# Performance work log

Hardware: AMD Instinct MI355X
Metric: run time of the kernel (lower is better)

## Reference

```python
import jax, jax.numpy as jnp
import numpy as np


def setup_inputs() -> dict:
    key = jax.random.key(0)
    ks = jax.random.split(key, 8)
    B, L, I, H, O = 512, 512, 256, 1024, 1
    def glorot(k, shape, fan_sum):
        return jax.random.uniform(k, shape, jnp.float32, -1.0, 1.0) * (6.0 / fan_sum) ** 0.5
    return {
        "X": jax.random.normal(ks[0], (B, L, I), jnp.float32),
        "W_in1": glorot(ks[1], (H, I), H + I),
        "b_in1": jnp.zeros((H, 1), jnp.float32),
        "W_rec1": glorot(ks[2], (H, H), H + H),
        "W_in2": glorot(ks[3], (H, I), H + I),
        "b_in2": jnp.zeros((H, 1), jnp.float32),
        "W_rec2": glorot(ks[4], (H, H), H + H),
        "W_out": glorot(ks[5], (O, H), O + H),
        "b_out": jnp.zeros((O, 1), jnp.float32),
    }


def reference(X, W_in1, b_in1, W_rec1, W_in2, b_in2, W_rec2, W_out, b_out):
    B, L, I = X.shape
    H = W_in1.shape[0]
    Xs = jnp.swapaxes(X, 0, 1)  # (L, B, I)
    # Precompute the input-to-hidden projections for all timesteps (parallel GEMMs).
    in1 = jnp.einsum("hi,lbi->lbh", W_in1, Xs) + b_in1[:, 0]  # (L, B, H)
    in2 = jnp.einsum("hi,lbi->lbh", W_in2, Xs) + b_in2[:, 0]  # (L, B, H)
    even = (jnp.arange(L) % 2 == 0)[:, None, None]  # (L, 1, 1) broadcast mask

    def step(carry, xs):
        z12, z1, z2 = carry  # each (B, H)
        a1, a2, ev = xs
        z1n = jnp.tanh(a1 + z12 @ W_rec1.T)
        z2n = jnp.where(ev, jnp.tanh(a2 + z2 @ W_rec2.T), z2)  # branch updates only on even l
        return (z1n + z2n, z1n, z2n), None

    z0 = jnp.zeros((B, H), X.dtype)
    (z12, z1, z2), _ = jax.lax.scan(step, (z0, z0, z0), (in1, in2, even))
    z_out = jnp.tanh(z1 @ W_out.T + b_out[:, 0])  # (B, num_outputs)
    return z_out.reshape(B, 1)
```

## Files before the change

### kernel.cpp

```cpp
#include <hip/hip_runtime.h>
#include <hip/hip_bf16.h>

typedef __attribute__((ext_vector_type(8))) short bhalf8;
typedef __attribute__((ext_vector_type(4))) float fvec4;
typedef __attribute__((ext_vector_type(4))) unsigned u32x4;

static __device__ __forceinline__ unsigned short f2bf(float f) {
  unsigned u = __builtin_bit_cast(unsigned, f);
  u = (u + 0x7fffu + ((u >> 16) & 1u)) >> 16;
  return (unsigned short)u;
}
static __device__ __forceinline__ float tanh_fast(float x) {
  x = fminf(12.f, fmaxf(-12.f, x));
  float e = __expf(2.f * x);
  return (e - 1.f) / (e + 1.f);
}
static __device__ __forceinline__ fvec4 tanh4(fvec4 v) {
  fvec4 r;
  r[0] = tanh_fast(v[0]); r[1] = tanh_fast(v[1]);
  r[2] = tanh_fast(v[2]); r[3] = tanh_fast(v[3]);
  return r;
}
static __device__ __forceinline__ bhalf8 load_w8(const float* p) {
  fvec4 a = *(const fvec4*)p;
  fvec4 b = *(const fvec4*)(p + 4);
  bhalf8 r;
  r[0] = (short)f2bf(a[0]); r[1] = (short)f2bf(a[1]);
  r[2] = (short)f2bf(a[2]); r[3] = (short)f2bf(a[3]);
  r[4] = (short)f2bf(b[0]); r[5] = (short)f2bf(b[1]);
  r[6] = (short)f2bf(b[2]); r[7] = (short)f2bf(b[3]);
  return r;
}

static __device__ __forceinline__ void st_short_coh(unsigned short* p, unsigned v) {
  asm volatile("global_store_short %0, %1, off sc0 sc1" :: "v"(p), "v"(v) : "memory");
}
static __device__ __forceinline__ void st_f32_coh(float* p, float v) {
  asm volatile("global_store_dword %0, %1, off sc0 sc1" :: "v"(p), "v"(v) : "memory");
}
static __device__ __forceinline__ void st_u32_coh(unsigned* p, unsigned v) {
  asm volatile("global_store_dword %0, %1, off sc0 sc1" :: "v"(p), "v"(v) : "memory");
}
static __device__ __forceinline__ u32x4 ld16_coh(const void* p) {
  u32x4 v;
  asm volatile("global_load_dwordx4 %0, %1, off sc0 sc1" : "=v"(v) : "v"(p) : "memory");
  return v;
}
static __device__ __forceinline__ unsigned ld_u32_coh(const unsigned* p) {
  unsigned v;
  asm volatile("global_load_dword %0, %1, off sc0 sc1\n\ts_waitcnt vmcnt(0)"
               : "=v"(v) : "v"(p) : "memory");
  return v;
}
static __device__ __forceinline__ float ld_f32_coh(const float* p) {
  float v;
  asm volatile("global_load_dword %0, %1, off sc0 sc1\n\ts_waitcnt vmcnt(0)"
               : "=v"(v) : "v"(p) : "memory");
  return v;
}

#define MFMA16(a, b, c) __builtin_amdgcn_mfma_f32_16x16x32_bf16((a), (b), (c), 0, 0, 0)

extern "C" __global__ void __launch_bounds__(256, 1)
alarm_rnn_persist(const float* __restrict__ X, const float* __restrict__ Win1,
                  const float* __restrict__ bin1, const float* __restrict__ Wrec1,
                  const float* __restrict__ Win2, const float* __restrict__ bin2,
                  const float* __restrict__ Wrec2, const float* __restrict__ Wout,
                  const float* __restrict__ bout, float* __restrict__ out,
                  unsigned* flags, unsigned short* gbuf0, unsigned short* gbuf1,
                  unsigned short* z2b0, unsigned short* z2b1, float* z1buf)
{
  constexpr int kL = 512, kI = 256, kH = 1024;
  extern __shared__ char smem[];

  const int tid = threadIdx.x, bid = blockIdx.x;
  const int grp = bid >> 4, memb = bid & 15;
  const int lane = tid & 63;
  const int row16 = lane & 15, kq = lane >> 4;
  const int hcol = memb * 64 + (tid >> 6) * 16 + row16;
  const int brow0 = grp * 32;

  bhalf8 w1[32], w2[32], wi1[8], wi2[8];
  {
    const float* p1 = Wrec1 + (size_t)hcol * kH + kq * 8;
    const float* p2 = Wrec2 + (size_t)hcol * kH + kq * 8;
#pragma unroll
    for (int kk = 0; kk < 32; ++kk) {
      w1[kk] = load_w8(p1 + kk * 32);
      w2[kk] = load_w8(p2 + kk * 32);
    }
    const float* q1 = Win1 + (size_t)hcol * kI + kq * 8;
    const float* q2 = Win2 + (size_t)hcol * kI + kq * 8;
#pragma unroll
    for (int kk = 0; kk < 8; ++kk) {
      wi1[kk] = load_w8(q1 + kk * 32);
      wi2[kk] = load_w8(q2 + kk * 32);
    }
  }
  const float bv1 = bin1[hcol];
  const float bv2 = bin2[hcol];
  fvec4 z2r0 = {0.f, 0.f, 0.f, 0.f}, z2r1 = {0.f, 0.f, 0.f, 0.f};

  {
    int r = tid >> 3, q = tid & 7;
    const float* xp = X + (size_t)(brow0 + r) * (kL * kI);
    fvec4 xv[8];
#pragma unroll
    for (int j = 0; j < 8; ++j) xv[j] = *(const fvec4*)(xp + q * 4 + j * 32);
#pragma unroll
    for (int j = 0; j < 8; ++j) {
      int i0 = q * 4 + j * 32;
      ushort4 pk;
      pk.x = f2bf(xv[j][0]); pk.y = f2bf(xv[j][1]);
      pk.z = f2bf(xv[j][2]); pk.w = f2bf(xv[j][3]);
      *(ushort4*)(smem + 65536 + (r << 9) + ((i0 * 2) ^ ((r & 7) << 4))) = pk;
    }
  }

  for (int l = 0; l < kL; ++l) {
    const bool even = ((l & 1) == 0);
    const int e = l >> 1;

    {
      const unsigned short* zsrc = (l & 1) ? gbuf1 : gbuf0;
      u32x4 tmp[16];
#pragma unroll
      for (int it = 0; it < 16; ++it) {
        int c = it * 256 + tid;
        int r = c >> 7, cb = (c & 127) * 16;
        tmp[it] = ld16_coh((const char*)zsrc + (((size_t)(brow0 + r)) << 11) + cb);
      }
      asm volatile("s_waitcnt vmcnt(0)" ::: "memory");
      __builtin_amdgcn_sched_barrier(0);
#pragma unroll
      for (int it = 0; it < 16; ++it) {
        int c = it * 256 + tid;
        int r = c >> 7, cb = (c & 127) * 16;
        *(u32x4*)(smem + (r << 11) + (cb ^ ((r & 7) << 4))) = tmp[it];
      }
    }
    if (even) {
      const unsigned short* z2src = (e & 1) ? z2b1 : z2b0;
      u32x4 tmp[16];
#pragma unroll
      for (int it = 0; it < 16; ++it) {
        int c = it * 256 + tid;
        int r = c >> 7, cb = (c & 127) * 16;
        tmp[it] = ld16_coh((const char*)z2src + (((size_t)(brow0 + r)) << 11) + cb);
      }
      asm volatile("s_waitcnt vmcnt(0)" ::: "memory");
      __builtin_amdgcn_sched_barrier(0);
#pragma unroll
      for (int it = 0; it < 16; ++it) {
        int c = it * 256 + tid;
        int r = c >> 7, cb = (c & 127) * 16;
        *(u32x4*)(smem + 81920 + (r << 11) + (cb ^ ((r & 7) << 4))) = tmp[it];
      }
    }
    __syncthreads();

    const int sw = (row16 & 7) << 4;

    fvec4 acc0 = {bv1, bv1, bv1, bv1}, acc1 = acc0;
#pragma unroll
    for (int kk = 0; kk < 8; ++kk) {
      int cb = kk * 64 + kq * 16;
      bhalf8 a0 = *(const bhalf8*)(smem + 65536 + (row16 << 9) + (cb ^ sw));
      bhalf8 a1 = *(const bhalf8*)(smem + 65536 + ((16 + row16) << 9) + (cb ^ sw));
      acc0 = MFMA16(a0, wi1[kk], acc0);
      acc1 = MFMA16(a1, wi1[kk], acc1);
    }
#pragma unroll
    for (int kk = 0; kk < 32; ++kk) {
      int cb = kk * 64 + kq * 16;
      bhalf8 a0 = *(const bhalf8*)(smem + (row16 << 11) + (cb ^ sw));
      bhalf8 a1 = *(const bhalf8*)(smem + ((16 + row16) << 11) + (cb ^ sw));
      acc0 = MFMA16(a0, w1[kk], acc0);
      acc1 = MFMA16(a1, w1[kk], acc1);
    }
    fvec4 z1n0 = tanh4(acc0), z1n1 = tanh4(acc1);

    if (even) {
      fvec4 bacc0 = {bv2, bv2, bv2, bv2}, bacc1 = bacc0;
#pragma unroll
      for (int kk = 0; kk < 8; ++kk) {
        int cb = kk * 64 + kq * 16;
        bhalf8 a0 = *(const bhalf8*)(smem + 65536 + (row16 << 9) + (cb ^ sw));
        bhalf8 a1 = *(const bhalf8*)(smem + 65536 + ((16 + row16) << 9) + (cb ^ sw));
        bacc0 = MFMA16(a0, wi2[kk], bacc0);
        bacc1 = MFMA16(a1, wi2[kk], bacc1);
      }
#pragma unroll
      for (int kk = 0; kk < 32; ++kk) {
        int cb = kk * 64 + kq * 16;
        bhalf8 a0 = *(const bhalf8*)(smem + 81920 + (row16 << 11) + (cb ^ sw));
        bhalf8 a1 = *(const bhalf8*)(smem + 81920 + ((16 + row16) << 11) + (cb ^ sw));
        bacc0 = MFMA16(a0, w2[kk], bacc0);
        bacc1 = MFMA16(a1, w2[kk], bacc1);
      }
      z2r0 = tanh4(bacc0);
      z2r1 = tanh4(bacc1);
      unsigned short* z2dst = (e & 1) ? z2b0 : z2b1;
#pragma unroll
      for (int i = 0; i < 4; ++i) {
        st_short_coh(z2dst + (size_t)(brow0 + kq * 4 + i) * kH + hcol, f2bf(z2r0[i]));
        st_short_coh(z2dst + (size_t)(brow0 + 16 + kq * 4 + i) * kH + hcol, f2bf(z2r1[i]));
      }
    }

    if (l < kL - 1) {
      unsigned short* dst = (l & 1) ? gbuf0 : gbuf1;
#pragma unroll
      for (int i = 0; i < 4; ++i) {
        st_short_coh(dst + (size_t)(brow0 + kq * 4 + i) * kH + hcol, f2bf(z1n0[i] + z2r0[i]));
        st_short_coh(dst + (size_t)(brow0 + 16 + kq * 4 + i) * kH + hcol, f2bf(z1n1[i] + z2r1[i]));
      }
    } else {
#pragma unroll
      for (int i = 0; i < 4; ++i) {
        st_f32_coh(z1buf + (size_t)(brow0 + kq * 4 + i) * kH + hcol, z1n0[i]);
        st_f32_coh(z1buf + (size_t)(brow0 + 16 + kq * 4 + i) * kH + hcol, z1n1[i]);
      }
    }

    asm volatile("s_waitcnt vmcnt(0)" ::: "memory");
    __syncthreads();
    if (tid == 0) st_u32_coh(flags + grp * 16 + memb, (unsigned)(l + 1));

    fvec4 xv[8];
    const int xr = tid >> 3, xq = tid & 7;
    if (l + 1 < kL) {
      const float* xp = X + (size_t)(brow0 + xr) * (kL * kI) + (size_t)(l + 1) * kI;
#pragma unroll
      for (int j = 0; j < 8; ++j) xv[j] = *(const fvec4*)(xp + xq * 4 + j * 32);
    }

    {
      const unsigned tgt = (unsigned)(l + 1);
      const unsigned* fp = flags + grp * 16 + (lane & 15);
      for (;;) {
        unsigned v = (lane < 16) ? ld_u32_coh(fp) : tgt;
        bool ok = (lane >= 16) || ((lane & 15) == memb) || (v >= tgt);
        if (__all(ok)) break;
        __builtin_amdgcn_s_sleep(1);
      }
      __builtin_amdgcn_sched_barrier(0);
    }

    if (l + 1 < kL) {
#pragma unroll
      for (int j = 0; j < 8; ++j) {
        int i0 = xq * 4 + j * 32;
        ushort4 pk;
        pk.x = f2bf(xv[j][0]); pk.y = f2bf(xv[j][1]);
        pk.z = f2bf(xv[j][2]); pk.w = f2bf(xv[j][3]);
        *(ushort4*)(smem + 65536 + (xr << 9) + ((i0 * 2) ^ ((xr & 7) << 4))) = pk;
      }
    }
  }

  if (memb == 0) {
    int r = tid >> 3, q = tid & 7;
    const float* zr = z1buf + (size_t)(brow0 + r) * kH;
    float s = 0.f;
    for (int h = q * 128; h < q * 128 + 128; ++h) s += ld_f32_coh(zr + h) * Wout[h];
    s += __shfl_xor(s, 1);
    s += __shfl_xor(s, 2);
    s += __shfl_xor(s, 4);
    if (q == 0) out[brow0 + r] = tanh_fast(s + bout[0]);
  }
}

extern "C" void kernel_launch(void* const* d_in, const int* in_sizes, int n_in,
                              void* d_out, int out_size, void* d_ws, size_t ws_size,
                              hipStream_t stream) {
  const float* X = (const float*)d_in[0];
  const float* Win1 = (const float*)d_in[1];
  const float* bin1 = (const float*)d_in[2];
  const float* Wrec1 = (const float*)d_in[3];
  const float* Win2 = (const float*)d_in[4];
  const float* bin2 = (const float*)d_in[5];
  const float* Wrec2 = (const float*)d_in[6];
  const float* Wout = (const float*)d_in[7];
  const float* bout = (const float*)d_in[8];
  float* out = (float*)d_out;

  char* ws = (char*)d_ws;
  unsigned* flags = (unsigned*)ws;
  unsigned short* gbuf0 = (unsigned short*)(ws + 4096);
  unsigned short* gbuf1 = (unsigned short*)(ws + 4096 + (1 << 20));
  unsigned short* z2b0 = (unsigned short*)(ws + 4096 + (2 << 20));
  unsigned short* z2b1 = (unsigned short*)(ws + 4096 + (3 << 20));
  float* z1buf = (float*)(ws + 4096 + (4 << 20));

  (void)hipMemsetAsync(flags, 0, 4096, stream);
  (void)hipMemsetAsync(gbuf0, 0, (size_t)512 * 1024 * 2, stream);
  (void)hipMemsetAsync(z2b0, 0, (size_t)512 * 1024 * 2, stream);

  (void)hipFuncSetAttribute((const void*)alarm_rnn_persist,
                            hipFuncAttributeMaxDynamicSharedMemorySize, 147456);

  alarm_rnn_persist<<<dim3(256), dim3(256), 147456, stream>>>(
      X, Win1, bin1, Wrec1, Win2, bin2, Wrec2, Wout, bout, out,
      flags, gbuf0, gbuf1, z2b0, z2b1, z1buf);
}
```

Before: 6.243 ms.

## Move branch-2 recurrence off critical path into post-flag slack of odd steps

The z2 branch update for the next even step is now computed during odd steps, after the step's flag is published and before the spin-wait. This hides branch-2 work behind the cross-block barrier latency. The first z2 is computed before the loop from the input projection alone, since z2 starts at zero. X slices are double-buffered two steps ahead, and the z1 input-projection MFMAs overlap the global load of the recurrent state. Shared memory grows to 160 KB and the z2 memset is removed.

```diff
diff --git a/kernel.cpp b/kernel.cpp
--- a/kernel.cpp
+++ b/kernel.cpp
@@ -77,6 +77,7 @@
   const int grp = bid >> 4, memb = bid & 15;
   const int lane = tid & 63;
   const int row16 = lane & 15, kq = lane >> 4;
+  const int sw = (row16 & 7) << 4;
   const int hcol = memb * 64 + (tid >> 6) * 16 + row16;
   const int brow0 = grp * 32;
 
@@ -99,77 +100,78 @@
   }
   const float bv1 = bin1[hcol];
   const float bv2 = bin2[hcol];
-  fvec4 z2r0 = {0.f, 0.f, 0.f, 0.f}, z2r1 = {0.f, 0.f, 0.f, 0.f};
 
   {
     int r = tid >> 3, q = tid & 7;
-    const float* xp = X + (size_t)(brow0 + r) * (kL * kI);
-    fvec4 xv[8];
-#pragma unroll
-    for (int j = 0; j < 8; ++j) xv[j] = *(const fvec4*)(xp + q * 4 + j * 32);
-#pragma unroll
-    for (int j = 0; j < 8; ++j) {
-      int i0 = q * 4 + j * 32;
-      ushort4 pk;
-      pk.x = f2bf(xv[j][0]); pk.y = f2bf(xv[j][1]);
-      pk.z = f2bf(xv[j][2]); pk.w = f2bf(xv[j][3]);
-      *(ushort4*)(smem + 65536 + (r << 9) + ((i0 * 2) ^ ((r & 7) << 4))) = pk;
-    }
-  }
-
-  for (int l = 0; l < kL; ++l) {
-    const bool even = ((l & 1) == 0);
-    const int e = l >> 1;
-
-    {
-      const unsigned short* zsrc = (l & 1) ? gbuf1 : gbuf0;
-      u32x4 tmp[16];
-#pragma unroll
-      for (int it = 0; it < 16; ++it) {
-        int c = it * 256 + tid;
-        int r = c >> 7, cb = (c & 127) * 16;
-        tmp[it] = ld16_coh((const char*)zsrc + (((size_t)(brow0 + r)) << 11) + cb);
-      }
-      asm volatile("s_waitcnt vmcnt(0)" ::: "memory");
-      __builtin_amdgcn_sched_barrier(0);
-#pragma unroll
-      for (int it = 0; it < 16; ++it) {
-        int c = it * 256 + tid;
-        int r = c >> 7, cb = (c & 127) * 16;
-        *(u32x4*)(smem + (r << 11) + (cb ^ ((r & 7) << 4))) = tmp[it];
-      }
-    }
-    if (even) {
-      const unsigned short* z2src = (e & 1) ? z2b1 : z2b0;
-      u32x4 tmp[16];
-#pragma unroll
-      for (int it = 0; it < 16; ++it) {
-        int c = it * 256 + tid;
-        int r = c >> 7, cb = (c & 127) * 16;
-        tmp[it] = ld16_coh((const char*)z2src + (((size_t)(brow0 + r)) << 11) + cb);
-      }
-      asm volatile("s_waitcnt vmcnt(0)" ::: "memory");
-      __builtin_amdgcn_sched_barrier(0);
-#pragma unroll
-      for (int it = 0; it < 16; ++it) {
-        int c = it * 256 + tid;
-        int r = c >> 7, cb = (c & 127) * 16;
-        *(u32x4*)(smem + 81920 + (r << 11) + (cb ^ ((r & 7) << 4))) = tmp[it];
-      }
-    }
-    __syncthreads();
-
-    const int sw = (row16 & 7) << 4;
-
-    fvec4 acc0 = {bv1, bv1, bv1, bv1}, acc1 = acc0;
+#pragma unroll
+    for (int p = 0; p < 2; ++p) {
+      const float* xp = X + (size_t)(brow0 + r) * (kL * kI) + (size_t)p * kI;
+      fvec4 xv[8];
+#pragma unroll
+      for (int j = 0; j < 8; ++j) xv[j] = *(const fvec4*)(xp + q * 4 + j * 32);
+#pragma unroll
+      for (int j = 0; j < 8; ++j) {
+        int i0 = q * 4 + j * 32;
+        ushort4 pk;
+        pk.x = f2bf(xv[j][0]); pk.y = f2bf(xv[j][1]);
+        pk.z = f2bf(xv[j][2]); pk.w = f2bf(xv[j][3]);
+        *(ushort4*)(smem + 65536 + p * 16384 + (r << 9) + ((i0 * 2) ^ ((r & 7) << 4))) = pk;
+      }
+    }
+  }
+  __syncthreads();
+  fvec4 z2c0, z2c1;
+  {
+    fvec4 b0 = {bv2, bv2, bv2, bv2}, b1 = b0;
 #pragma unroll
     for (int kk = 0; kk < 8; ++kk) {
       int cb = kk * 64 + kq * 16;
       bhalf8 a0 = *(const bhalf8*)(smem + 65536 + (row16 << 9) + (cb ^ sw));
       bhalf8 a1 = *(const bhalf8*)(smem + 65536 + ((16 + row16) << 9) + (cb ^ sw));
+      b0 = MFMA16(a0, wi2[kk], b0);
+      b1 = MFMA16(a1, wi2[kk], b1);
+    }
+    z2c0 = tanh4(b0);
+    z2c1 = tanh4(b1);
+#pragma unroll
+    for (int i = 0; i < 4; ++i) {
+      st_short_coh(z2b0 + (size_t)(brow0 + kq * 4 + i) * kH + hcol, f2bf(z2c0[i]));
+      st_short_coh(z2b0 + (size_t)(brow0 + 16 + kq * 4 + i) * kH + hcol, f2bf(z2c1[i]));
+    }
+  }
+
+  for (int l = 0; l < kL; ++l) {
+    u32x4 ztmp[16];
+    {
+      const unsigned short* zsrc = (l & 1) ? gbuf1 : gbuf0;
+#pragma unroll
+      for (int it = 0; it < 16; ++it) {
+        int c = it * 256 + tid;
+        int r = c >> 7, cb = (c & 127) * 16;
+        ztmp[it] = ld16_coh((const char*)zsrc + (((size_t)(brow0 + r)) << 11) + cb);
+      }
+    }
+    const char* xb = smem + 65536 + ((l & 1) << 14);
+    fvec4 acc0 = {bv1, bv1, bv1, bv1}, acc1 = acc0;
+#pragma unroll
+    for (int kk = 0; kk < 8; ++kk) {
+      int cb = kk * 64 + kq * 16;
+      bhalf8 a0 = *(const bhalf8*)(xb + (row16 << 9) + (cb ^ sw));
+      bhalf8 a1 = *(const bhalf8*)(xb + ((16 + row16) << 9) + (cb ^ sw));
       acc0 = MFMA16(a0, wi1[kk], acc0);
       acc1 = MFMA16(a1, wi1[kk], acc1);
     }
+    __builtin_amdgcn_sched_barrier(0);
+    asm volatile("s_waitcnt vmcnt(0)" ::: "memory");
+    __builtin_amdgcn_sched_barrier(0);
+#pragma unroll
+    for (int it = 0; it < 16; ++it) {
+      int c = it * 256 + tid;
+      int r = c >> 7, cb = (c & 127) * 16;
+      *(u32x4*)(smem + (r << 11) + (cb ^ ((r & 7) << 4))) = ztmp[it];
+    }
+    __syncthreads();
+
 #pragma unroll
     for (int kk = 0; kk < 32; ++kk) {
       int cb = kk * 64 + kq * 16;
@@ -180,40 +182,12 @@
     }
     fvec4 z1n0 = tanh4(acc0), z1n1 = tanh4(acc1);
 
-    if (even) {
-      fvec4 bacc0 = {bv2, bv2, bv2, bv2}, bacc1 = bacc0;
-#pragma unroll
-      for (int kk = 0; kk < 8; ++kk) {
-        int cb = kk * 64 + kq * 16;
-        bhalf8 a0 = *(const bhalf8*)(smem + 65536 + (row16 << 9) + (cb ^ sw));
-        bhalf8 a1 = *(const bhalf8*)(smem + 65536 + ((16 + row16) << 9) + (cb ^ sw));
-        bacc0 = MFMA16(a0, wi2[kk], bacc0);
-        bacc1 = MFMA16(a1, wi2[kk], bacc1);
-      }
-#pragma unroll
-      for (int kk = 0; kk < 32; ++kk) {
-        int cb = kk * 64 + kq * 16;
-        bhalf8 a0 = *(const bhalf8*)(smem + 81920 + (row16 << 11) + (cb ^ sw));
-        bhalf8 a1 = *(const bhalf8*)(smem + 81920 + ((16 + row16) << 11) + (cb ^ sw));
-        bacc0 = MFMA16(a0, w2[kk], bacc0);
-        bacc1 = MFMA16(a1, w2[kk], bacc1);
-      }
-      z2r0 = tanh4(bacc0);
-      z2r1 = tanh4(bacc1);
-      unsigned short* z2dst = (e & 1) ? z2b0 : z2b1;
-#pragma unroll
-      for (int i = 0; i < 4; ++i) {
-        st_short_coh(z2dst + (size_t)(brow0 + kq * 4 + i) * kH + hcol, f2bf(z2r0[i]));
-        st_short_coh(z2dst + (size_t)(brow0 + 16 + kq * 4 + i) * kH + hcol, f2bf(z2r1[i]));
-      }
-    }
-
     if (l < kL - 1) {
       unsigned short* dst = (l & 1) ? gbuf0 : gbuf1;
 #pragma unroll
       for (int i = 0; i < 4; ++i) {
-        st_short_coh(dst + (size_t)(brow0 + kq * 4 + i) * kH + hcol, f2bf(z1n0[i] + z2r0[i]));
-        st_short_coh(dst + (size_t)(brow0 + 16 + kq * 4 + i) * kH + hcol, f2bf(z1n1[i] + z2r1[i]));
+        st_short_coh(dst + (size_t)(brow0 + kq * 4 + i) * kH + hcol, f2bf(z1n0[i] + z2c0[i]));
+        st_short_coh(dst + (size_t)(brow0 + 16 + kq * 4 + i) * kH + hcol, f2bf(z1n1[i] + z2c1[i]));
       }
     } else {
 #pragma unroll
@@ -222,17 +196,83 @@
         st_f32_coh(z1buf + (size_t)(brow0 + 16 + kq * 4 + i) * kH + hcol, z1n1[i]);
       }
     }
-
     asm volatile("s_waitcnt vmcnt(0)" ::: "memory");
     __syncthreads();
     if (tid == 0) st_u32_coh(flags + grp * 16 + memb, (unsigned)(l + 1));
 
     fvec4 xv[8];
     const int xr = tid >> 3, xq = tid & 7;
-    if (l + 1 < kL) {
-      const float* xp = X + (size_t)(brow0 + xr) * (kL * kI) + (size_t)(l + 1) * kI;
+    if (l + 2 < kL) {
+      const float* xp = X + (size_t)(brow0 + xr) * (kL * kI) + (size_t)(l + 2) * kI;
 #pragma unroll
       for (int j = 0; j < 8; ++j) xv[j] = *(const fvec4*)(xp + xq * 4 + j * 32);
+    }
+
+    if ((l & 1) && l < kL - 1) {
+      const int e = (l - 1) >> 1;
+      const unsigned short* z2src = (e & 1) ? z2b1 : z2b0;
+      u32x4 zt[16];
+#pragma unroll
+      for (int it = 0; it < 16; ++it) {
+        int c = it * 256 + tid;
+        int r = c >> 7, cb = (c & 127) * 16;
+        zt[it] = ld16_coh((const char*)z2src + (((size_t)(brow0 + r)) << 11) + cb);
+      }
+      const char* xb1 = smem + 65536 + (((l + 1) & 1) << 14);
+      fvec4 b0 = {bv2, bv2, bv2, bv2}, b1 = b0;
+#pragma unroll
+      for (int kk = 0; kk < 8; ++kk) {
+        int cb = kk * 64 + kq * 16;
+        bhalf8 a0 = *(const bhalf8*)(xb1 + (row16 << 9) + (cb ^ sw));
+        bhalf8 a1 = *(const bhalf8*)(xb1 + ((16 + row16) << 9) + (cb ^ sw));
+        b0 = MFMA16(a0, wi2[kk], b0);
+        b1 = MFMA16(a1, wi2[kk], b1);
+      }
+      __builtin_amdgcn_sched_barrier(0);
+      asm volatile("s_waitcnt vmcnt(0)" ::: "memory");
+      __builtin_amdgcn_sched_barrier(0);
+#pragma unroll
+      for (int it = 0; it < 16; ++it) {
+        int c = it * 256 + tid;
+        int r = c >> 7, cb = (c & 127) * 16;
+        *(u32x4*)(smem + 98304 + (r << 11) + (cb ^ ((r & 7) << 4))) = zt[it];
+      }
+      if (l + 2 < kL) {
+#pragma unroll
+        for (int j = 0; j < 8; ++j) {
+          int i0 = xq * 4 + j * 32;
+          ushort4 pk;
+          pk.x = f2bf(xv[j][0]); pk.y = f2bf(xv[j][1]);
+          pk.z = f2bf(xv[j][2]); pk.w = f2bf(xv[j][3]);
+          *(ushort4*)(smem + 65536 + ((l & 1) << 14) + (xr << 9) + ((i0 * 2) ^ ((xr & 7) << 4))) = pk;
+        }
+      }
+      __syncthreads();
+#pragma unroll
+      for (int kk = 0; kk < 32; ++kk) {
+        int cb = kk * 64 + kq * 16;
+        bhalf8 a0 = *(const bhalf8*)(smem + 98304 + (row16 << 11) + (cb ^ sw));
+        bhalf8 a1 = *(const bhalf8*)(smem + 98304 + ((16 + row16) << 11) + (cb ^ sw));
+        b0 = MFMA16(a0, w2[kk], b0);
+        b1 = MFMA16(a1, w2[kk], b1);
+      }
+      z2c0 = tanh4(b0);
+      z2c1 = tanh4(b1);
+      unsigned short* z2dst = ((e + 1) & 1) ? z2b1 : z2b0;
+#pragma unroll
+      for (int i = 0; i < 4; ++i) {
+        st_short_coh(z2dst + (size_t)(brow0 + kq * 4 + i) * kH + hcol, f2bf(z2c0[i]));
+        st_short_coh(z2dst + (size_t)(brow0 + 16 + kq * 4 + i) * kH + hcol, f2bf(z2c1[i]));
+      }
+    } else if (l + 2 < kL) {
+#pragma unroll
+      for (int j = 0; j < 8; ++j) {
+        int i0 = xq * 4 + j * 32;
+        ushort4 pk;
+        pk.x = f2bf(xv[j][0]); pk.y = f2bf(xv[j][1]);
+        pk.z = f2bf(xv[j][2]); pk.w = f2bf(xv[j][3]);
+        *(ushort4*)(smem + 65536 + ((l & 1) << 14) + (xr << 9) + ((i0 * 2) ^ ((xr & 7) << 4))) = pk;
+      }
     }
 
     {
@@ -245,17 +285,6 @@
         __builtin_amdgcn_s_sleep(1);
       }
       __builtin_amdgcn_sched_barrier(0);
-    }
-
-    if (l + 1 < kL) {
-#pragma unroll
-      for (int j = 0; j < 8; ++j) {
-        int i0 = xq * 4 + j * 32;
-        ushort4 pk;
-        pk.x = f2bf(xv[j][0]); pk.y = f2bf(xv[j][1]);
-        pk.z = f2bf(xv[j][2]); pk.w = f2bf(xv[j][3]);
-        *(ushort4*)(smem + 65536 + (xr << 9) + ((i0 * 2) ^ ((xr & 7) << 4))) = pk;
-      }
     }
   }
 
@@ -295,12 +324,11 @@
 
   (void)hipMemsetAsync(flags, 0, 4096, stream);
   (void)hipMemsetAsync(gbuf0, 0, (size_t)512 * 1024 * 2, stream);
-  (void)hipMemsetAsync(z2b0, 0, (size_t)512 * 1024 * 2, stream);
 
   (void)hipFuncSetAttribute((const void*)alarm_rnn_persist,
-                            hipFuncAttributeMaxDynamicSharedMemorySize, 147456);
-
-  alarm_rnn_persist<<<dim3(256), dim3(256), 147456, stream>>>(
+                            hipFuncAttributeMaxDynamicSharedMemorySize, 163840);
+
+  alarm_rnn_persist<<<dim3(256), dim3(256), 163840, stream>>>(
       X, Win1, bin1, Wrec1, Win2, bin2, Wrec2, Wout, bout, out,
       flags, gbuf0, gbuf1, z2b0, z2b1, z1buf);
 }
```

Result: slower. 7.094 ms (+13.6%).

## Use direct global-to-LDS loads and overlap input projections with state fetch

Applied to the files above, without the earlier changes.

Replaces the register-staged coherent loads of the hidden state with global_load_lds into swizzled LDS, issued asynchronously. While those loads are in flight, the input-projection MFMAs for both branches are computed from a double-buffered X tile. The X tile for step l+2 is now prefetched and converted before the flag spin-wait rather than after it. This moves the input GEMM off the critical path after synchronisation, at the cost of more LDS (160KB) and reliance on correct swizzling with per-lane LDS placement.

```diff
diff --git a/kernel.cpp b/kernel.cpp
--- a/kernel.cpp
+++ b/kernel.cpp
@@ -3,7 +3,6 @@
 
 typedef __attribute__((ext_vector_type(8))) short bhalf8;
 typedef __attribute__((ext_vector_type(4))) float fvec4;
-typedef __attribute__((ext_vector_type(4))) unsigned u32x4;
 
 static __device__ __forceinline__ unsigned short f2bf(float f) {
   unsigned u = __builtin_bit_cast(unsigned, f);
@@ -41,11 +40,6 @@
 static __device__ __forceinline__ void st_u32_coh(unsigned* p, unsigned v) {
   asm volatile("global_store_dword %0, %1, off sc0 sc1" :: "v"(p), "v"(v) : "memory");
 }
-static __device__ __forceinline__ u32x4 ld16_coh(const void* p) {
-  u32x4 v;
-  asm volatile("global_load_dwordx4 %0, %1, off sc0 sc1" : "=v"(v) : "v"(p) : "memory");
-  return v;
-}
 static __device__ __forceinline__ unsigned ld_u32_coh(const unsigned* p) {
   unsigned v;
   asm volatile("global_load_dword %0, %1, off sc0 sc1\n\ts_waitcnt vmcnt(0)"
@@ -57,6 +51,11 @@
   asm volatile("global_load_dword %0, %1, off sc0 sc1\n\ts_waitcnt vmcnt(0)"
                : "=v"(v) : "v"(p) : "memory");
   return v;
+}
+static __device__ __forceinline__ void gll16_coh(const void* g, void* lds) {
+  __builtin_amdgcn_global_load_lds(
+      (const __attribute__((address_space(1))) void*)g,
+      (__attribute__((address_space(3))) void*)lds, 16, 0, 0x11);
 }
 
 #define MFMA16(a, b, c) __builtin_amdgcn_mfma_f32_16x16x32_bf16((a), (b), (c), 0, 0, 0)
@@ -75,9 +74,10 @@
 
   const int tid = threadIdx.x, bid = blockIdx.x;
   const int grp = bid >> 4, memb = bid & 15;
-  const int lane = tid & 63;
+  const int lane = tid & 63, w = tid >> 6;
   const int row16 = lane & 15, kq = lane >> 4;
-  const int hcol = memb * 64 + (tid >> 6) * 16 + row16;
+  const int sw = (row16 & 7) << 4;
+  const int hcol = memb * 64 + w * 16 + row16;
   const int brow0 = grp * 32;
 
   bhalf8 w1[32], w2[32], wi1[8], wi2[8];
@@ -99,23 +99,27 @@
   }
   const float bv1 = bin1[hcol];
   const float bv2 = bin2[hcol];
-  fvec4 z2r0 = {0.f, 0.f, 0.f, 0.f}, z2r1 = {0.f, 0.f, 0.f, 0.f};
+  fvec4 z2c0 = {0.f, 0.f, 0.f, 0.f}, z2c1 = {0.f, 0.f, 0.f, 0.f};
 
   {
     int r = tid >> 3, q = tid & 7;
-    const float* xp = X + (size_t)(brow0 + r) * (kL * kI);
-    fvec4 xv[8];
-#pragma unroll
-    for (int j = 0; j < 8; ++j) xv[j] = *(const fvec4*)(xp + q * 4 + j * 32);
-#pragma unroll
-    for (int j = 0; j < 8; ++j) {
-      int i0 = q * 4 + j * 32;
-      ushort4 pk;
-      pk.x = f2bf(xv[j][0]); pk.y = f2bf(xv[j][1]);
-      pk.z = f2bf(xv[j][2]); pk.w = f2bf(xv[j][3]);
-      *(ushort4*)(smem + 65536 + (r << 9) + ((i0 * 2) ^ ((r & 7) << 4))) = pk;
-    }
-  }
+#pragma unroll
+    for (int p = 0; p < 2; ++p) {
+      const float* xp = X + (size_t)(brow0 + r) * (kL * kI) + (size_t)p * kI;
+      fvec4 xv[8];
+#pragma unroll
+      for (int j = 0; j < 8; ++j) xv[j] = *(const fvec4*)(xp + q * 4 + j * 32);
+#pragma unroll
+      for (int j = 0; j < 8; ++j) {
+        int i0 = q * 4 + j * 32;
+        ushort4 pk;
+        pk.x = f2bf(xv[j][0]); pk.y = f2bf(xv[j][1]);
+        pk.z = f2bf(xv[j][2]); pk.w = f2bf(xv[j][3]);
+        *(ushort4*)(smem + 131072 + p * 16384 + (r << 9) + ((i0 * 2) ^ ((r & 7) << 4))) = pk;
+      }
+    }
+  }
+  __syncthreads();
 
   for (int l = 0; l < kL; ++l) {
     const bool even = ((l & 1) == 0);
@@ -123,53 +127,51 @@
 
     {
       const unsigned short* zsrc = (l & 1) ? gbuf1 : gbuf0;
-      u32x4 tmp[16];
 #pragma unroll
       for (int it = 0; it < 16; ++it) {
-        int c = it * 256 + tid;
-        int r = c >> 7, cb = (c & 127) * 16;
-        tmp[it] = ld16_coh((const char*)zsrc + (((size_t)(brow0 + r)) << 11) + cb);
-      }
-      asm volatile("s_waitcnt vmcnt(0)" ::: "memory");
+        int c = ((it * 4 + w) << 6) + lane;
+        int r = c >> 7, cbs = (c & 127) * 16;
+        gll16_coh((const char*)zsrc + (((size_t)(brow0 + r)) << 11) + (cbs ^ ((r & 7) << 4)),
+                  smem + ((it * 4 + w) << 10));
+      }
+      if (even) {
+        const unsigned short* z2src = (e & 1) ? z2b1 : z2b0;
+#pragma unroll
+        for (int it = 0; it < 16; ++it) {
+          int c = ((it * 4 + w) << 6) + lane;
+          int r = c >> 7, cbs = (c & 127) * 16;
+          gll16_coh((const char*)z2src + (((size_t)(brow0 + r)) << 11) + (cbs ^ ((r & 7) << 4)),
+                    smem + 65536 + ((it * 4 + w) << 10));
+        }
+      }
       __builtin_amdgcn_sched_barrier(0);
-#pragma unroll
-      for (int it = 0; it < 16; ++it) {
-        int c = it * 256 + tid;
-        int r = c >> 7, cb = (c & 127) * 16;
-        *(u32x4*)(smem + (r << 11) + (cb ^ ((r & 7) << 4))) = tmp[it];
-      }
-    }
-    if (even) {
-      const unsigned short* z2src = (e & 1) ? z2b1 : z2b0;
-      u32x4 tmp[16];
-#pragma unroll
-      for (int it = 0; it < 16; ++it) {
-        int c = it * 256 + tid;
-        int r = c >> 7, cb = (c & 127) * 16;
-        tmp[it] = ld16_coh((const char*)z2src + (((size_t)(brow0 + r)) << 11) + cb);
-      }
-      asm volatile("s_waitcnt vmcnt(0)" ::: "memory");
-      __builtin_amdgcn_sched_barrier(0);
-#pragma unroll
-      for (int it = 0; it < 16; ++it) {
-        int c = it * 256 + tid;
-        int r = c >> 7, cb = (c & 127) * 16;
-        *(u32x4*)(smem + 81920 + (r << 11) + (cb ^ ((r & 7) << 4))) = tmp[it];
-      }
-    }
-    __syncthreads();
-
-    const int sw = (row16 & 7) << 4;
-
+    }
+
+    const char* xb = smem + 131072 + ((l & 1) << 14);
     fvec4 acc0 = {bv1, bv1, bv1, bv1}, acc1 = acc0;
 #pragma unroll
     for (int kk = 0; kk < 8; ++kk) {
       int cb = kk * 64 + kq * 16;
-      bhalf8 a0 = *(const bhalf8*)(smem + 65536 + (row16 << 9) + (cb ^ sw));
-      bhalf8 a1 = *(const bhalf8*)(smem + 65536 + ((16 + row16) << 9) + (cb ^ sw));
+      bhalf8 a0 = *(const bhalf8*)(xb + (row16 << 9) + (cb ^ sw));
+      bhalf8 a1 = *(const bhalf8*)(xb + ((16 + row16) << 9) + (cb ^ sw));
       acc0 = MFMA16(a0, wi1[kk], acc0);
       acc1 = MFMA16(a1, wi1[kk], acc1);
     }
+    fvec4 c2a0 = {bv2, bv2, bv2, bv2}, c2a1 = c2a0;
+    if (even) {
+#pragma unroll
+      for (int kk = 0; kk < 8; ++kk) {
+        int cb = kk * 64 + kq * 16;
+        bhalf8 a0 = *(const bhalf8*)(xb + (row16 << 9) + (cb ^ sw));
+        bhalf8 a1 = *(const bhalf8*)(xb + ((16 + row16) << 9) + (cb ^ sw));
+        c2a0 = MFMA16(a0, wi2[kk], c2a0);
+        c2a1 = MFMA16(a1, wi2[kk], c2a1);
+      }
+    }
+    asm volatile("s_waitcnt vmcnt(0)" ::: "memory");
+    __builtin_amdgcn_sched_barrier(0);
+    __syncthreads();
+
 #pragma unroll
     for (int kk = 0; kk < 32; ++kk) {
       int cb = kk * 64 + kq * 16;
@@ -181,39 +183,24 @@
     fvec4 z1n0 = tanh4(acc0), z1n1 = tanh4(acc1);
 
     if (even) {
-      fvec4 bacc0 = {bv2, bv2, bv2, bv2}, bacc1 = bacc0;
-#pragma unroll
-      for (int kk = 0; kk < 8; ++kk) {
-        int cb = kk * 64 + kq * 16;
-        bhalf8 a0 = *(const bhalf8*)(smem + 65536 + (row16 << 9) + (cb ^ sw));
-        bhalf8 a1 = *(const bhalf8*)(smem + 65536 + ((16 + row16) << 9) + (cb ^ sw));
-        bacc0 = MFMA16(a0, wi2[kk], bacc0);
-        bacc1 = MFMA16(a1, wi2[kk], bacc1);
-      }
 #pragma unroll
       for (int kk = 0; kk < 32; ++kk) {
         int cb = kk * 64 + kq * 16;
-        bhalf8 a0 = *(const bhalf8*)(smem + 81920 + (row16 << 11) + (cb ^ sw));
-        bhalf8 a1 = *(const bhalf8*)(smem + 81920 + ((16 + row16) << 11) + (cb ^ sw));
-        bacc0 = MFMA16(a0, w2[kk], bacc0);
-        bacc1 = MFMA16(a1, w2[kk], bacc1);
-      }
-      z2r0 = tanh4(bacc0);
-      z2r1 = tanh4(bacc1);
-      unsigned short* z2dst = (e & 1) ? z2b0 : z2b1;
-#pragma unroll
-      for (int i = 0; i < 4; ++i) {
-        st_short_coh(z2dst + (size_t)(brow0 + kq * 4 + i) * kH + hcol, f2bf(z2r0[i]));
-        st_short_coh(z2dst + (size_t)(brow0 + 16 + kq * 4 + i) * kH + hcol, f2bf(z2r1[i]));
-      }
+        bhalf8 a0 = *(const bhalf8*)(smem + 65536 + (row16 << 11) + (cb ^ sw));
+        bhalf8 a1 = *(const bhalf8*)(smem + 65536 + ((16 + row16) << 11) + (cb ^ sw));
+        c2a0 = MFMA16(a0, w2[kk], c2a0);
+        c2a1 = MFMA16(a1, w2[kk], c2a1);
+      }
+      z2c0 = tanh4(c2a0);
+      z2c1 = tanh4(c2a1);
     }
 
     if (l < kL - 1) {
       unsigned short* dst = (l & 1) ? gbuf0 : gbuf1;
 #pragma unroll
       for (int i = 0; i < 4; ++i) {
-        st_short_coh(dst + (size_t)(brow0 + kq * 4 + i) * kH + hcol, f2bf(z1n0[i] + z2r0[i]));
-        st_short_coh(dst + (size_t)(brow0 + 16 + kq * 4 + i) * kH + hcol, f2bf(z1n1[i] + z2r1[i]));
+        st_short_coh(dst + (size_t)(brow0 + kq * 4 + i) * kH + hcol, f2bf(z1n0[i] + z2c0[i]));
+        st_short_coh(dst + (size_t)(brow0 + 16 + kq * 4 + i) * kH + hcol, f2bf(z1n1[i] + z2c1[i]));
       }
     } else {
 #pragma unroll
@@ -222,17 +209,32 @@
         st_f32_coh(z1buf + (size_t)(brow0 + 16 + kq * 4 + i) * kH + hcol, z1n1[i]);
       }
     }
-
+    if (even) {
+      unsigned short* z2dst = (e & 1) ? z2b0 : z2b1;
+#pragma unroll
+      for (int i = 0; i < 4; ++i) {
+        st_short_coh(z2dst + (size_t)(brow0 + kq * 4 + i) * kH + hcol, f2bf(z2c0[i]));
+        st_short_coh(z2dst + (size_t)(brow0 + 16 + kq * 4 + i) * kH + hcol, f2bf(z2c1[i]));
+      }
+    }
     asm volatile("s_waitcnt vmcnt(0)" ::: "memory");
     __syncthreads();
     if (tid == 0) st_u32_coh(flags + grp * 16 + memb, (unsigned)(l + 1));
 
-    fvec4 xv[8];
-    const int xr = tid >> 3, xq = tid & 7;
-    if (l + 1 < kL) {
-      const float* xp = X + (size_t)(brow0 + xr) * (kL * kI) + (size_t)(l + 1) * kI;
+    if (l + 2 < kL) {
+      const int xr = tid >> 3, xq = tid & 7;
+      const float* xp = X + (size_t)(brow0 + xr) * (kL * kI) + (size_t)(l + 2) * kI;
+      fvec4 xv[8];
 #pragma unroll
       for (int j = 0; j < 8; ++j) xv[j] = *(const fvec4*)(xp + xq * 4 + j * 32);
+#pragma unroll
+      for (int j = 0; j < 8; ++j) {
+        int i0 = xq * 4 + j * 32;
+        ushort4 pk;
+        pk.x = f2bf(xv[j][0]); pk.y = f2bf(xv[j][1]);
+        pk.z = f2bf(xv[j][2]); pk.w = f2bf(xv[j][3]);
+        *(ushort4*)(smem + 131072 + ((l & 1) << 14) + (xr << 9) + ((i0 * 2) ^ ((xr & 7) << 4))) = pk;
+      }
     }
 
     {
@@ -245,17 +247,6 @@
         __builtin_amdgcn_s_sleep(1);
       }
       __builtin_amdgcn_sched_barrier(0);
-    }
-
-    if (l + 1 < kL) {
-#pragma unroll
-      for (int j = 0; j < 8; ++j) {
-        int i0 = xq * 4 + j * 32;
-        ushort4 pk;
-        pk.x = f2bf(xv[j][0]); pk.y = f2bf(xv[j][1]);
-        pk.z = f2bf(xv[j][2]); pk.w = f2bf(xv[j][3]);
-        *(ushort4*)(smem + 65536 + (xr << 9) + ((i0 * 2) ^ ((xr & 7) << 4))) = pk;
-      }
     }
   }
 
@@ -298,9 +289,9 @@
   (void)hipMemsetAsync(z2b0, 0, (size_t)512 * 1024 * 2, stream);
 
   (void)hipFuncSetAttribute((const void*)alarm_rnn_persist,
-                            hipFuncAttributeMaxDynamicSharedMemorySize, 147456);
-
-  alarm_rnn_persist<<<dim3(256), dim3(256), 147456, stream>>>(
+                            hipFuncAttributeMaxDynamicSharedMemorySize, 163840);
+
+  alarm_rnn_persist<<<dim3(256), dim3(256), 163840, stream>>>(
       X, Win1, bin1, Wrec1, Win2, bin2, Wrec2, Wout, bout, out,
       flags, gbuf0, gbuf1, z2b0, z2b1, z1buf);
 }
```

Result: slower. 6.382 ms (+2.2%).
